# Kernel optimization log

Hardware: AMD Instinct MI355X
Metric: run time of the kernel (lower is better)

The kernel has to match this reference:

```python
import jax, jax.numpy as jnp
import numpy as np

HEAD_DIM = 64
AGGR = 4  # attn_aggr_ratio
BN_EPS = 1e-5


def _conv1x1(x, W, b=None):
    # x: [N, Cin, L], W: [Cout, Cin] -> [N, Cout, L]
    y = jnp.einsum('ncl,oc->nol', x, W)
    if b is not None:
        y = y + b[None, :, None]
    return y


def _bn(x, gamma, beta, mean, var):
    # BatchNorm1d, eval mode (running stats). x: [N, C, L]
    inv = gamma * jax.lax.rsqrt(var + BN_EPS)
    return x * inv[None, :, None] + (beta - mean * inv)[None, :, None]


def setup_inputs() -> dict:
    key = jax.random.key(0)
    ks = jax.random.split(key, 8)
    N, C, L = 4, 256, 4096
    s = 1.0 / np.sqrt(C)
    inp = {
        'x': jax.random.normal(ks[0], (N, C, L), jnp.float32),
        'Wq': jax.random.normal(ks[1], (C, C), jnp.float32) * s,
        'bq': jnp.zeros((C,), jnp.float32),
        'Wk': jax.random.normal(ks[2], (C, C), jnp.float32) * s,
        'bk': jnp.zeros((C,), jnp.float32),
        'Wv': jax.random.normal(ks[3], (C, C), jnp.float32) * s,
        'bv': jnp.zeros((C,), jnp.float32),
        'Wo': jax.random.normal(ks[4], (C, C), jnp.float32) * s,
        'bo': jnp.zeros((C,), jnp.float32),
        'Wa': jax.random.normal(ks[5], (C, C), jnp.float32) * s,
        'g1': jnp.ones((C,), jnp.float32), 'b1': jnp.zeros((C,), jnp.float32),
        'm1': jnp.zeros((C,), jnp.float32), 'v1': jnp.ones((C,), jnp.float32),
        'g2': jnp.ones((C,), jnp.float32), 'b2': jnp.zeros((C,), jnp.float32),
        'm2': jnp.zeros((C,), jnp.float32), 'v2': jnp.ones((C,), jnp.float32),
    }
    return inp


def reference(x, Wq, bq, Wk, bk, Wv, bv, Wo, bo, Wa,
              g1, b1, m1, v1, g2, b2, m2, v2):
    N, C, L = x.shape
    H, E = C // HEAD_DIM, HEAD_DIM
    # q projection on full-resolution input
    q = _conv1x1(x, Wq, bq).reshape(N, H, E, L)
    # LocalAwareAggregationBlock: avg+max pool (kernel=AGGR, L divisible), 1x1 conv, BN
    xp = x.reshape(N, C, L // AGGR, AGGR)
    xa = xp.mean(axis=-1) + xp.max(axis=-1)          # [N, C, L//AGGR]
    xa = _conv1x1(xa, Wa)                             # bias=False
    xa = _bn(xa, g1, b1, m1, v1)
    # post-aggregation norm
    xa = _bn(xa, g2, b2, m2, v2)
    k = _conv1x1(xa, Wk, bk).reshape(N, H, E, -1)     # [N, H, E, L2]
    v = _conv1x1(xa, Wv, bv).reshape(N, H, E, -1)
    # attention: softmax((q/sqrt(E))^T k) @ v^T
    scale = 1.0 / np.sqrt(E)
    scores = jnp.einsum('nhel,nhem->nhlm', q * scale, k)  # [N, H, L, L2]
    attn = jax.nn.softmax(scores, axis=-1)
    o = jnp.einsum('nhlm,nhem->nhel', attn, v).reshape(N, C, L)
    return _conv1x1(o, Wo, bo)
```

## Files before the change

### kernel.cpp

```cpp
#include <hip/hip_runtime.h>
#include <stdint.h>

constexpr int NBATCH = 4;
constexpr int CH     = 256;
constexpr int LEN    = 4096;
constexpr int LPOOL  = 1024;
constexpr int NH     = 4;
constexpr int HD     = 64;

typedef __attribute__((ext_vector_type(8))) short short8;
typedef __attribute__((ext_vector_type(4))) float float4e;
typedef __attribute__((ext_vector_type(16))) float float16e;
typedef __attribute__((ext_vector_type(2))) unsigned uint2v;

__device__ __forceinline__ unsigned short f2bf(float f) {
    union { unsigned int i; float f; } v; v.f = f;
    unsigned int lsb = (v.i >> 16) & 1u;
    v.i += 0x7fffu + lsb;
    return (unsigned short)(v.i >> 16);
}
__device__ __forceinline__ unsigned pack2bf(float lo, float hi) {
    unsigned a = __float_as_uint(lo) + 0x8000u;
    unsigned b = __float_as_uint(hi) + 0x8000u;
    return __builtin_amdgcn_perm(b, a, 0x07060302u);
}
__device__ __forceinline__ float fast_exp2(float x) {
#if __has_builtin(__builtin_amdgcn_exp2f)
    return __builtin_amdgcn_exp2f(x);
#else
    float r;
    asm("v_exp_f32 %0, %1" : "=v"(r) : "v"(x));
    return r;
#endif
}
__device__ __forceinline__ void gload16(const void* g, void* l) {
    __builtin_amdgcn_global_load_lds(
        (const __attribute__((address_space(1))) unsigned int*)g,
        (__attribute__((address_space(3))) unsigned int*)l, 16, 0, 0);
}

__global__ __launch_bounds__(256) void transpool_setup(
    const float* __restrict__ x, unsigned short* __restrict__ xbf,
    unsigned short* __restrict__ poolT,
    const float* __restrict__ w0, const float* __restrict__ w1,
    const float* __restrict__ w2, const float* __restrict__ w3,
    const float* __restrict__ w4, unsigned short* __restrict__ outW,
    const float* __restrict__ g1, const float* __restrict__ b1,
    const float* __restrict__ m1, const float* __restrict__ v1,
    const float* __restrict__ g2, const float* __restrict__ b2,
    const float* __restrict__ m2, const float* __restrict__ v2,
    float* __restrict__ scale, float* __restrict__ shift,
    const float* __restrict__ bk, const float* __restrict__ bv,
    float* __restrict__ bkv)
{
    __shared__ float T[64][65];
    __shared__ float P16[64][17];
    int b = blockIdx.x, t = threadIdx.x;
    if (b >= 1024) {
        int sb = b - 1024;
        if (sb < 320) {
            int gid = sb * 256 + t;
            int w = gid >> 14;
            int off = (gid & 16383) * 4;
            const float* src = (w == 0) ? w0 : (w == 1) ? w1 : (w == 2) ? w2 : (w == 3) ? w3 : w4;
            float4 v = *(const float4*)(src + off);
            uint2 pk;
            pk.x = pack2bf(v.x, v.y);
            pk.y = pack2bf(v.z, v.w);
            *(uint2*)(outW + w * 65536 + off) = pk;
        } else {
            float inv1 = g1[t] * rsqrtf(v1[t] + 1e-5f);
            float inv2 = g2[t] * rsqrtf(v2[t] + 1e-5f);
            scale[t] = inv1 * inv2;
            shift[t] = (b1[t] - m1[t] * inv1) * inv2 + (b2[t] - m2[t] * inv2);
            bkv[t] = bk[t];
            bkv[256 + t] = bv[t];
        }
        return;
    }
    int n = b >> 8, c0 = ((b >> 6) & 3) * 64, l0 = (b & 63) * 64;
    const float* xp = x + ((size_t)n * CH + c0) * LEN + l0;
    #pragma unroll
    for (int i = 0; i < 4; i++) {
        int idx = t + i * 256;
        int c = idx >> 4, l4 = idx & 15;
        float4 v = *(const float4*)(xp + (size_t)c * LEN + l4 * 4);
        T[c][l4 * 4 + 0] = v.x; T[c][l4 * 4 + 1] = v.y;
        T[c][l4 * 4 + 2] = v.z; T[c][l4 * 4 + 3] = v.w;
        P16[c][l4] = (v.x + v.y + v.z + v.w) * 0.25f
                   + fmaxf(fmaxf(v.x, v.y), fmaxf(v.z, v.w));
    }
    __syncthreads();
    unsigned short* op = xbf + ((size_t)n * LEN + l0) * CH + c0;
    #pragma unroll
    for (int i = 0; i < 4; i++) {
        int idx = t + i * 256;
        int l = idx >> 4, c4 = idx & 15;
        uint2 pk;
        pk.x = pack2bf(T[c4 * 4 + 0][l], T[c4 * 4 + 1][l]);
        pk.y = pack2bf(T[c4 * 4 + 2][l], T[c4 * 4 + 3][l]);
        *(uint2*)(op + (size_t)l * CH + c4 * 4) = pk;
    }
    int p0 = l0 >> 2;
    #pragma unroll
    for (int k = 0; k < 2; k++) {
        int p = (t >> 5) + k * 8;
        int c2 = (t & 31) * 2;
        unsigned pk = pack2bf(P16[c2][p], P16[c2 + 1][p]);
        *(unsigned*)(poolT + ((size_t)n * LPOOL + p0 + p) * CH + c0 + c2) = pk;
    }
}

__global__ __launch_bounds__(256) void gemm_mfma(
    const unsigned short* __restrict__ A,
    const unsigned short* __restrict__ B, size_t bBatch,
    const float* __restrict__ biasRow,
    const float* __restrict__ scale, const float* __restrict__ shift,
    float* __restrict__ outF, size_t oFBatch,
    unsigned short* __restrict__ out1, size_t o1Batch, int cs1,
    unsigned short* __restrict__ out2, size_t o2Batch, int rs2, int rowSplit,
    int NN, float outScale)
{
    __shared__ unsigned short smem[2 * 128 * 72];
    unsigned short* As = smem;
    unsigned short* Bs = smem + 128 * 72;

    int n = blockIdx.z;
    int t = threadIdx.x;
    int wave = t >> 6, lane = t & 63, m = lane & 15, quad = lane >> 4;
    int wm = wave & 1, wn = wave >> 1;
    int rowTile = blockIdx.y * 128;
    int col0 = blockIdx.x * 128;

    const unsigned short* Ab = A + (size_t)rowTile * 256;
    const unsigned short* Bb = B + (size_t)n * bBatch + (size_t)col0 * 256;

    float4e acc[4][4] = {};

    for (int kk = 0; kk < 256; kk += 64) {
        #pragma unroll
        for (int i = 0; i < 4; i++) {
            int idx = t + i * 256;
            int row = idx >> 3, ch = idx & 7;
            *(uint4*)&As[row * 72 + ch * 8] = *(const uint4*)(Ab + (size_t)row * 256 + kk + ch * 8);
            *(uint4*)&Bs[row * 72 + ch * 8] = *(const uint4*)(Bb + (size_t)row * 256 + kk + ch * 8);
        }
        __syncthreads();
        #pragma unroll
        for (int kc = 0; kc < 2; kc++) {
            short8 af[4], bfr[4];
            #pragma unroll
            for (int i = 0; i < 4; i++)
                af[i] = *(const short8*)&As[(wm * 64 + i * 16 + m) * 72 + kc * 32 + quad * 8];
            #pragma unroll
            for (int j = 0; j < 4; j++)
                bfr[j] = *(const short8*)&Bs[(wn * 64 + j * 16 + m) * 72 + kc * 32 + quad * 8];
            #pragma unroll
            for (int i = 0; i < 4; i++)
                #pragma unroll
                for (int j = 0; j < 4; j++)
                    acc[i][j] = __builtin_amdgcn_mfma_f32_16x16x32_bf16(af[i], bfr[j], acc[i][j], 0, 0, 0);
        }
        __syncthreads();
    }

    if (outF) {
        float* TOf = (float*)smem;
        float* dst = outF + (size_t)n * oFBatch;
        #pragma unroll
        for (int half = 0; half < 2; half++) {
            __syncthreads();
            if (wm == half) {
                #pragma unroll
                for (int i = 0; i < 4; i++) {
                    int rowL = i * 16 + quad * 4;
                    int rowG = rowTile + half * 64 + rowL;
                    float br[4], sc[4], sh[4];
                    #pragma unroll
                    for (int r = 0; r < 4; r++) {
                        br[r] = biasRow ? biasRow[rowG + r] : 0.0f;
                        sc[r] = scale ? scale[rowG + r] : 1.0f;
                        sh[r] = shift ? shift[rowG + r] : 0.0f;
                    }
                    #pragma unroll
                    for (int j = 0; j < 4; j++) {
                        int colL = wn * 64 + j * 16 + m;
                        float4e c = acc[i][j];
                        #pragma unroll
                        for (int r = 0; r < 4; r++)
                            TOf[(rowL + r) * 128 + colL] = ((c[r] + br[r]) * sc[r] + sh[r]) * outScale;
                    }
                }
            }
            __syncthreads();
            #pragma unroll
            for (int w = 0; w < 8; w++) {
                int idx = t + w * 256;
                int row = idx >> 5, c4 = idx & 31;
                *(float4*)(dst + (size_t)(rowTile + half * 64 + row) * NN + col0 + c4 * 4) =
                    *(const float4*)&TOf[row * 128 + c4 * 4];
            }
        }
        return;
    }

    bool mode2 = (rowTile >= rowSplit);
    unsigned short* TO = smem;
    #pragma unroll
    for (int i = 0; i < 4; i++) {
        int rowL = wm * 64 + i * 16 + quad * 4;
        int rowG = rowTile + rowL;
        float br[4], sc[4], sh[4];
        #pragma unroll
        for (int r = 0; r < 4; r++) {
            br[r] = biasRow ? biasRow[rowG + r] : 0.0f;
            sc[r] = scale ? scale[rowG + r] : 1.0f;
            sh[r] = shift ? shift[rowG + r] : 0.0f;
        }
        #pragma unroll
        for (int j = 0; j < 4; j++) {
            int colL = wn * 64 + j * 16 + m;
            float4e c = acc[i][j];
            float v0 = ((c[0] + br[0]) * sc[0] + sh[0]) * outScale;
            float v1 = ((c[1] + br[1]) * sc[1] + sh[1]) * outScale;
            float v2 = ((c[2] + br[2]) * sc[2] + sh[2]) * outScale;
            float v3 = ((c[3] + br[3]) * sc[3] + sh[3]) * outScale;
            if (!mode2) {
                uint2 pk;
                pk.x = pack2bf(v0, v1);
                pk.y = pack2bf(v2, v3);
                *(uint2*)&TO[colL * 136 + rowL] = pk;
            } else {
                TO[(rowL + 0) * 136 + colL] = f2bf(v0);
                TO[(rowL + 1) * 136 + colL] = f2bf(v1);
                TO[(rowL + 2) * 136 + colL] = f2bf(v2);
                TO[(rowL + 3) * 136 + colL] = f2bf(v3);
            }
        }
    }
    __syncthreads();
    if (!mode2) {
        unsigned short* dst = out1 + (size_t)n * o1Batch;
        #pragma unroll
        for (int w = 0; w < 8; w++) {
            int idx = t + w * 256;
            int l = idx >> 4, ch = idx & 15;
            *(uint4*)(dst + (size_t)(col0 + l) * cs1 + rowTile + ch * 8) =
                *(const uint4*)&TO[l * 136 + ch * 8];
        }
    } else {
        unsigned short* dst = out2 + (size_t)n * o2Batch;
        int rowBase = rowTile - rowSplit;
        #pragma unroll
        for (int w = 0; w < 8; w++) {
            int idx = t + w * 256;
            int row = idx >> 4, ch = idx & 15;
            *(uint4*)(dst + (size_t)(rowBase + row) * rs2 + col0 + ch * 8) =
                *(const uint4*)&TO[row * 136 + ch * 8];
        }
    }
}

__global__ __launch_bounds__(256, 2) void attn_mfma(
    const unsigned short* __restrict__ Qb,
    const unsigned short* __restrict__ Kb,
    const unsigned short* __restrict__ Vb,
    unsigned short* __restrict__ Obf)
{
    __shared__ unsigned short Ks[2][64 * 64];
    __shared__ unsigned short Vs[2][64 * 64];

    int qb = blockIdx.x;
    int h  = blockIdx.y;
    int n  = blockIdx.z;
    int t  = threadIdx.x;
    int wave = t >> 6, lane = t & 63;
    int col = lane & 31;
    int hi  = lane >> 5;
    int l0 = qb * 128 + wave * 32;

    const unsigned short* qp = Qb + ((size_t)n * LEN + l0 + col) * CH + h * HD + hi * 8;
    short8 bQ[4];
    #pragma unroll
    for (int dc = 0; dc < 4; dc++)
        bQ[dc] = *(const short8*)(qp + dc * 16);

    float16e Oa[2];
    #pragma unroll
    for (int e = 0; e < 2; e++)
        #pragma unroll
        for (int r = 0; r < 16; r++) Oa[e][r] = 0.0f;
    float l_run = 0.0f;

    const unsigned short* KgBase = Kb + (size_t)n * LPOOL * CH + h * HD;
    const unsigned short* VgBase = Vb + ((size_t)n * CH + h * HD) * LPOOL;
    const float NEG = -17.312340f;

    int srow[2], schs[2], ldsb[2];
    #pragma unroll
    for (int i = 0; i < 2; i++) {
        int idx = t + i * 256;
        srow[i] = idx >> 3;
        schs[i] = (idx & 7) ^ (srow[i] & 7);
        ldsb[i] = wave * 1024 + i * 4096;
    }
    int ldoff[2][4];
    #pragma unroll
    for (int g = 0; g < 2; g++)
        #pragma unroll
        for (int c = 0; c < 4; c++) {
            int row = g * 32 + col;
            ldoff[g][c] = row * 128 + ((c * 32 + hi * 16) ^ ((row & 7) << 4));
        }

    #pragma unroll
    for (int i = 0; i < 2; i++) {
        gload16(KgBase + (size_t)srow[i] * CH + schs[i] * 8, (char*)Ks[0] + ldsb[i]);
        gload16(VgBase + (size_t)srow[i] * LPOOL + schs[i] * 8, (char*)Vs[0] + ldsb[i]);
    }

    #pragma unroll 2
    for (int kt = 0; kt < 16; kt++) {
        int cur = kt & 1;
        asm volatile("s_waitcnt vmcnt(0)" ::: "memory");
        __builtin_amdgcn_sched_barrier(0);
        __builtin_amdgcn_s_barrier();
        __builtin_amdgcn_sched_barrier(0);
        if (kt < 15) {
            int nxt = cur ^ 1;
            const unsigned short* ksrc = KgBase + (size_t)(kt + 1) * 64 * CH;
            const unsigned short* vsrc = VgBase + (kt + 1) * 64;
            #pragma unroll
            for (int i = 0; i < 2; i++) {
                gload16(ksrc + (size_t)srow[i] * CH + schs[i] * 8, (char*)Ks[nxt] + ldsb[i]);
                gload16(vsrc + (size_t)srow[i] * LPOOL + schs[i] * 8, (char*)Vs[nxt] + ldsb[i]);
            }
        }

        const char* KsC = (const char*)Ks[cur];
        const char* VsC = (const char*)Vs[cur];
        #pragma unroll
        for (int kh = 0; kh < 2; kh++) {
            float16e c;
            #pragma unroll
            for (int r = 0; r < 16; r++) c[r] = NEG;
            __builtin_amdgcn_s_setprio(1);
            #pragma unroll
            for (int dc = 0; dc < 4; dc++) {
                short8 a = *(const short8*)(KsC + ldoff[kh][dc]);
                c = __builtin_amdgcn_mfma_f32_32x32x16_bf16(a, bQ[dc], c, 0, 0, 0);
            }
            __builtin_amdgcn_s_setprio(0);
            float p[16];
            #pragma unroll
            for (int r = 0; r < 16; r++) p[r] = fast_exp2(c[r]);
            l_run += ((p[0] + p[1]) + (p[2] + p[3])) + ((p[4] + p[5]) + (p[6] + p[7]))
                   + ((p[8] + p[9]) + (p[10] + p[11])) + ((p[12] + p[13]) + (p[14] + p[15]));
            union { unsigned u[4]; short8 s; } bP[2];
            #pragma unroll
            for (int kc2 = 0; kc2 < 2; kc2++) {
                int rb = kc2 * 8;
                unsigned A0 = pack2bf(p[rb + 0], p[rb + 1]);
                unsigned B0 = pack2bf(p[rb + 4], p[rb + 5]);
                unsigned A1 = pack2bf(p[rb + 2], p[rb + 3]);
                unsigned B1 = pack2bf(p[rb + 6], p[rb + 7]);
                uint2v s0 = __builtin_amdgcn_permlane32_swap(A0, B0, false, false);
                uint2v s1 = __builtin_amdgcn_permlane32_swap(A1, B1, false, false);
                bP[kc2].u[0] = s0[0];
                bP[kc2].u[1] = s1[0];
                bP[kc2].u[2] = s0[1];
                bP[kc2].u[3] = s1[1];
            }
            __builtin_amdgcn_s_setprio(1);
            #pragma unroll
            for (int eh = 0; eh < 2; eh++)
                #pragma unroll
                for (int kc2 = 0; kc2 < 2; kc2++) {
                    short8 av = *(const short8*)(VsC + ldoff[eh][kh * 2 + kc2]);
                    Oa[eh] = __builtin_amdgcn_mfma_f32_32x32x16_bf16(av, bP[kc2].s, Oa[eh], 0, 0, 0);
                }
            __builtin_amdgcn_s_setprio(0);
        }
    }

    float l = l_run + __shfl_xor(l_run, 32);
    float inv = 1.0f / l;
    unsigned short* op = Obf + ((size_t)n * LEN + l0 + col) * CH + h * HD + hi * 4;
    #pragma unroll
    for (int eh = 0; eh < 2; eh++)
        #pragma unroll
        for (int rq = 0; rq < 4; rq++) {
            int r = rq * 4;
            uint2 pk;
            pk.x = pack2bf(Oa[eh][r + 0] * inv, Oa[eh][r + 1] * inv);
            pk.y = pack2bf(Oa[eh][r + 2] * inv, Oa[eh][r + 3] * inv);
            *(uint2*)(op + eh * 32 + rq * 8) = pk;
        }
}

extern "C" void kernel_launch(void* const* d_in, const int* in_sizes, int n_in,
                              void* d_out, int out_size, void* d_ws, size_t ws_size,
                              hipStream_t stream)
{
    const float* x  = (const float*)d_in[0];
    const float* Wq = (const float*)d_in[1];
    const float* bq = (const float*)d_in[2];
    const float* Wk = (const float*)d_in[3];
    const float* bk = (const float*)d_in[4];
    const float* Wv = (const float*)d_in[5];
    const float* bv = (const float*)d_in[6];
    const float* Wo = (const float*)d_in[7];
    const float* bo = (const float*)d_in[8];
    const float* Wa = (const float*)d_in[9];
    const float* g1 = (const float*)d_in[10];
    const float* b1 = (const float*)d_in[11];
    const float* m1 = (const float*)d_in[12];
    const float* v1 = (const float*)d_in[13];
    const float* g2 = (const float*)d_in[14];
    const float* b2 = (const float*)d_in[15];
    const float* m2 = (const float*)d_in[16];
    const float* v2 = (const float*)d_in[17];

    float* wsf      = (float*)d_ws;
    float* bn_scale = wsf;
    float* bn_shift = wsf + 256;
    float* bkv      = wsf + 512;
    unsigned short* Wbf   = (unsigned short*)(wsf + 1024);
    unsigned short* xbf   = Wbf + 5 * 65536;
    unsigned short* poolT = xbf   + (size_t)NBATCH * LEN * CH;
    unsigned short* xabf  = poolT + (size_t)NBATCH * LPOOL * CH;
    unsigned short* Kbf   = xabf  + (size_t)NBATCH * LPOOL * CH;
    unsigned short* Vbf   = Kbf   + (size_t)NBATCH * LPOOL * CH;
    unsigned short* Qbf   = Vbf   + (size_t)NBATCH * LPOOL * CH;
    unsigned short* Obf   = Qbf   + (size_t)NBATCH * LEN * CH;

    transpool_setup<<<1345, 256, 0, stream>>>(x, xbf, poolT,
        Wq, Wk, Wv, Wo, Wa, Wbf,
        g1, b1, m1, v1, g2, b2, m2, v2, bn_scale, bn_shift, bk, bv, bkv);

    gemm_mfma<<<dim3(32, 2, 4), 256, 0, stream>>>(
        Wbf + 0 * 65536, xbf, (size_t)LEN * CH, bq, nullptr, nullptr,
        nullptr, 0, Qbf, (size_t)LEN * CH, 256, nullptr, 0, 0, 1 << 30,
        LEN, 0.18033688f);

    gemm_mfma<<<dim3(8, 2, 4), 256, 0, stream>>>(
        Wbf + 4 * 65536, poolT, (size_t)LPOOL * CH, nullptr, bn_scale, bn_shift,
        nullptr, 0, xabf, (size_t)LPOOL * CH, 256, nullptr, 0, 0, 1 << 30,
        LPOOL, 1.0f);

    gemm_mfma<<<dim3(8, 4, 4), 256, 0, stream>>>(
        Wbf + 1 * 65536, xabf, (size_t)LPOOL * CH, bkv, nullptr, nullptr,
        nullptr, 0, Kbf, (size_t)LPOOL * CH, 256, Vbf, (size_t)LPOOL * CH, LPOOL, 256,
        LPOOL, 1.0f);

    attn_mfma<<<dim3(LEN / 128, NH, NBATCH), 256, 0, stream>>>(Qbf, Kbf, Vbf, Obf);

    gemm_mfma<<<dim3(32, 2, 4), 256, 0, stream>>>(
        Wbf + 3 * 65536, Obf, (size_t)LEN * CH, bo, nullptr, nullptr,
        (float*)d_out, (size_t)CH * LEN, nullptr, 0, 0, nullptr, 0, 0, 1 << 30,
        LEN, 1.0f);
}
```

Baseline: 168.8 us.

## Double-buffer GEMM with direct global-to-LDS loads and smaller 64-row tiles

Rewrites the projection GEMM kernel to use 64x128 output tiles instead of 128x128 and doubles the grid's row dimension. The K loop is double-buffered: it issues direct global-to-LDS loads for the next K slice while MFMAs run on the current one, and raises wave priority around the MFMA block. It also uses occupancy hint 2 and a dedicated output staging buffer. The aim is to hide global load latency and give more blocks for better CU fill. In exchange the LDS rows are unpadded, which may cause bank conflicts, and each B tile is reused across fewer rows.

Result: faster. 158.8 us (-6.0%).

```diff
diff --git a/kernel.cpp b/kernel.cpp
--- a/kernel.cpp
+++ b/kernel.cpp
@@ -111,7 +111,7 @@
     }
 }
 
-__global__ __launch_bounds__(256) void gemm_mfma(
+__global__ __launch_bounds__(256, 2) void gemm_mfma(
     const unsigned short* __restrict__ A,
     const unsigned short* __restrict__ B, size_t bBatch,
     const float* __restrict__ biasRow,
@@ -121,94 +121,140 @@
     unsigned short* __restrict__ out2, size_t o2Batch, int rs2, int rowSplit,
     int NN, float outScale)
 {
-    __shared__ unsigned short smem[2 * 128 * 72];
-    unsigned short* As = smem;
-    unsigned short* Bs = smem + 128 * 72;
+    __shared__ unsigned short As[2][64 * 64];
+    __shared__ unsigned short Bs[2][128 * 64];
+    __shared__ unsigned short TO[128 * 72];
 
     int n = blockIdx.z;
     int t = threadIdx.x;
     int wave = t >> 6, lane = t & 63, m = lane & 15, quad = lane >> 4;
     int wm = wave & 1, wn = wave >> 1;
-    int rowTile = blockIdx.y * 128;
+    int rowTile = blockIdx.y * 64;
     int col0 = blockIdx.x * 128;
 
     const unsigned short* Ab = A + (size_t)rowTile * 256;
     const unsigned short* Bb = B + (size_t)n * bBatch + (size_t)col0 * 256;
 
-    float4e acc[4][4] = {};
-
-    for (int kk = 0; kk < 256; kk += 64) {
-        #pragma unroll
-        for (int i = 0; i < 4; i++) {
-            int idx = t + i * 256;
-            int row = idx >> 3, ch = idx & 7;
-            *(uint4*)&As[row * 72 + ch * 8] = *(const uint4*)(Ab + (size_t)row * 256 + kk + ch * 8);
-            *(uint4*)&Bs[row * 72 + ch * 8] = *(const uint4*)(Bb + (size_t)row * 256 + kk + ch * 8);
-        }
-        __syncthreads();
+    float4e acc[2][4] = {};
+
+    int arow[2], ach[2];
+    #pragma unroll
+    for (int i = 0; i < 2; i++) {
+        int idx = t + i * 256;
+        arow[i] = idx >> 3;
+        ach[i]  = idx & 7;
+    }
+    int brow[4], bch[4];
+    #pragma unroll
+    for (int i = 0; i < 4; i++) {
+        int idx = t + i * 256;
+        brow[i] = idx >> 3;
+        bch[i]  = idx & 7;
+    }
+    int ldsW[4];
+    #pragma unroll
+    for (int i = 0; i < 4; i++) ldsW[i] = wave * 1024 + i * 4096;
+
+    int aoff[2][2], boff[4][2];
+    #pragma unroll
+    for (int i = 0; i < 2; i++) {
+        int r = wm * 32 + i * 16 + m;
+        #pragma unroll
+        for (int kc = 0; kc < 2; kc++)
+            aoff[i][kc] = r * 128 + kc * 64 + quad * 16;
+    }
+    #pragma unroll
+    for (int j = 0; j < 4; j++) {
+        int r = wn * 64 + j * 16 + m;
+        #pragma unroll
+        for (int kc = 0; kc < 2; kc++)
+            boff[j][kc] = r * 128 + kc * 64 + quad * 16;
+    }
+
+    #pragma unroll
+    for (int i = 0; i < 2; i++)
+        gload16(Ab + (size_t)arow[i] * 256 + ach[i] * 8, (char*)As[0] + ldsW[i]);
+    #pragma unroll
+    for (int i = 0; i < 4; i++)
+        gload16(Bb + (size_t)brow[i] * 256 + bch[i] * 8, (char*)Bs[0] + ldsW[i]);
+
+    #pragma unroll
+    for (int s = 0; s < 4; s++) {
+        int cur = s & 1;
+        asm volatile("s_waitcnt vmcnt(0)" ::: "memory");
+        __builtin_amdgcn_sched_barrier(0);
+        __builtin_amdgcn_s_barrier();
+        __builtin_amdgcn_sched_barrier(0);
+        if (s < 3) {
+            int nxt = cur ^ 1;
+            int kk = (s + 1) * 64;
+            #pragma unroll
+            for (int i = 0; i < 2; i++)
+                gload16(Ab + (size_t)arow[i] * 256 + kk + ach[i] * 8, (char*)As[nxt] + ldsW[i]);
+            #pragma unroll
+            for (int i = 0; i < 4; i++)
+                gload16(Bb + (size_t)brow[i] * 256 + kk + bch[i] * 8, (char*)Bs[nxt] + ldsW[i]);
+        }
+        const char* AsC = (const char*)As[cur];
+        const char* BsC = (const char*)Bs[cur];
         #pragma unroll
         for (int kc = 0; kc < 2; kc++) {
-            short8 af[4], bfr[4];
-            #pragma unroll
-            for (int i = 0; i < 4; i++)
-                af[i] = *(const short8*)&As[(wm * 64 + i * 16 + m) * 72 + kc * 32 + quad * 8];
+            short8 af[2], bfr[4];
+            #pragma unroll
+            for (int i = 0; i < 2; i++)
+                af[i] = *(const short8*)(AsC + aoff[i][kc]);
             #pragma unroll
             for (int j = 0; j < 4; j++)
-                bfr[j] = *(const short8*)&Bs[(wn * 64 + j * 16 + m) * 72 + kc * 32 + quad * 8];
-            #pragma unroll
-            for (int i = 0; i < 4; i++)
+                bfr[j] = *(const short8*)(BsC + boff[j][kc]);
+            __builtin_amdgcn_s_setprio(1);
+            #pragma unroll
+            for (int i = 0; i < 2; i++)
                 #pragma unroll
                 for (int j = 0; j < 4; j++)
                     acc[i][j] = __builtin_amdgcn_mfma_f32_16x16x32_bf16(af[i], bfr[j], acc[i][j], 0, 0, 0);
+            __builtin_amdgcn_s_setprio(0);
+        }
+    }
+    __syncthreads();
+
+    if (outF) {
+        float* TOf = (float*)Bs;
+        float* dst = outF + (size_t)n * oFBatch;
+        #pragma unroll
+        for (int i = 0; i < 2; i++) {
+            int rowL = wm * 32 + i * 16 + quad * 4;
+            int rowG = rowTile + rowL;
+            float br[4], sc[4], sh[4];
+            #pragma unroll
+            for (int r = 0; r < 4; r++) {
+                br[r] = biasRow ? biasRow[rowG + r] : 0.0f;
+                sc[r] = scale ? scale[rowG + r] : 1.0f;
+                sh[r] = shift ? shift[rowG + r] : 0.0f;
+            }
+            #pragma unroll
+            for (int j = 0; j < 4; j++) {
+                int colL = wn * 64 + j * 16 + m;
+                float4e c = acc[i][j];
+                #pragma unroll
+                for (int r = 0; r < 4; r++)
+                    TOf[(rowL + r) * 128 + colL] = ((c[r] + br[r]) * sc[r] + sh[r]) * outScale;
+            }
         }
         __syncthreads();
-    }
-
-    if (outF) {
-        float* TOf = (float*)smem;
-        float* dst = outF + (size_t)n * oFBatch;
-        #pragma unroll
-        for (int half = 0; half < 2; half++) {
-            __syncthreads();
-            if (wm == half) {
-                #pragma unroll
-                for (int i = 0; i < 4; i++) {
-                    int rowL = i * 16 + quad * 4;
-                    int rowG = rowTile + half * 64 + rowL;
-                    float br[4], sc[4], sh[4];
-                    #pragma unroll
-                    for (int r = 0; r < 4; r++) {
-                        br[r] = biasRow ? biasRow[rowG + r] : 0.0f;
-                        sc[r] = scale ? scale[rowG + r] : 1.0f;
-                        sh[r] = shift ? shift[rowG + r] : 0.0f;
-                    }
-                    #pragma unroll
-                    for (int j = 0; j < 4; j++) {
-                        int colL = wn * 64 + j * 16 + m;
-                        float4e c = acc[i][j];
-                        #pragma unroll
-                        for (int r = 0; r < 4; r++)
-                            TOf[(rowL + r) * 128 + colL] = ((c[r] + br[r]) * sc[r] + sh[r]) * outScale;
-                    }
-                }
-            }
-            __syncthreads();
-            #pragma unroll
-            for (int w = 0; w < 8; w++) {
-                int idx = t + w * 256;
-                int row = idx >> 5, c4 = idx & 31;
-                *(float4*)(dst + (size_t)(rowTile + half * 64 + row) * NN + col0 + c4 * 4) =
-                    *(const float4*)&TOf[row * 128 + c4 * 4];
-            }
+        #pragma unroll
+        for (int w = 0; w < 8; w++) {
+            int idx = t + w * 256;
+            int row = idx >> 5, c4 = idx & 31;
+            *(float4*)(dst + (size_t)(rowTile + row) * NN + col0 + c4 * 4) =
+                *(const float4*)&TOf[row * 128 + c4 * 4];
         }
         return;
     }
 
     bool mode2 = (rowTile >= rowSplit);
-    unsigned short* TO = smem;
-    #pragma unroll
-    for (int i = 0; i < 4; i++) {
-        int rowL = wm * 64 + i * 16 + quad * 4;
+    #pragma unroll
+    for (int i = 0; i < 2; i++) {
+        int rowL = wm * 32 + i * 16 + quad * 4;
         int rowG = rowTile + rowL;
         float br[4], sc[4], sh[4];
         #pragma unroll
@@ -229,7 +275,7 @@
                 uint2 pk;
                 pk.x = pack2bf(v0, v1);
                 pk.y = pack2bf(v2, v3);
-                *(uint2*)&TO[colL * 136 + rowL] = pk;
+                *(uint2*)&TO[colL * 72 + rowL] = pk;
             } else {
                 TO[(rowL + 0) * 136 + colL] = f2bf(v0);
                 TO[(rowL + 1) * 136 + colL] = f2bf(v1);
@@ -242,17 +288,17 @@
     if (!mode2) {
         unsigned short* dst = out1 + (size_t)n * o1Batch;
         #pragma unroll
-        for (int w = 0; w < 8; w++) {
+        for (int w = 0; w < 4; w++) {
             int idx = t + w * 256;
-            int l = idx >> 4, ch = idx & 15;
+            int l = idx >> 3, ch = idx & 7;
             *(uint4*)(dst + (size_t)(col0 + l) * cs1 + rowTile + ch * 8) =
-                *(const uint4*)&TO[l * 136 + ch * 8];
+                *(const uint4*)&TO[l * 72 + ch * 8];
         }
     } else {
         unsigned short* dst = out2 + (size_t)n * o2Batch;
         int rowBase = rowTile - rowSplit;
         #pragma unroll
-        for (int w = 0; w < 8; w++) {
+        for (int w = 0; w < 4; w++) {
             int idx = t + w * 256;
             int row = idx >> 4, ch = idx & 15;
             *(uint4*)(dst + (size_t)(rowBase + row) * rs2 + col0 + ch * 8) =
@@ -438,24 +484,24 @@
         Wq, Wk, Wv, Wo, Wa, Wbf,
         g1, b1, m1, v1, g2, b2, m2, v2, bn_scale, bn_shift, bk, bv, bkv);
 
-    gemm_mfma<<<dim3(32, 2, 4), 256, 0, stream>>>(
+    gemm_mfma<<<dim3(32, 4, 4), 256, 0, stream>>>(
         Wbf + 0 * 65536, xbf, (size_t)LEN * CH, bq, nullptr, nullptr,
         nullptr, 0, Qbf, (size_t)LEN * CH, 256, nullptr, 0, 0, 1 << 30,
         LEN, 0.18033688f);
 
-    gemm_mfma<<<dim3(8, 2, 4), 256, 0, stream>>>(
+    gemm_mfma<<<dim3(8, 4, 4), 256, 0, stream>>>(
         Wbf + 4 * 65536, poolT, (size_t)LPOOL * CH, nullptr, bn_scale, bn_shift,
         nullptr, 0, xabf, (size_t)LPOOL * CH, 256, nullptr, 0, 0, 1 << 30,
         LPOOL, 1.0f);
 
-    gemm_mfma<<<dim3(8, 4, 4), 256, 0, stream>>>(
+    gemm_mfma<<<dim3(8, 8, 4), 256, 0, stream>>>(
         Wbf + 1 * 65536, xabf, (size_t)LPOOL * CH, bkv, nullptr, nullptr,
         nullptr, 0, Kbf, (size_t)LPOOL * CH, 256, Vbf, (size_t)LPOOL * CH, LPOOL, 256,
         LPOOL, 1.0f);
 
     attn_mfma<<<dim3(LEN / 128, NH, NBATCH), 256, 0, stream>>>(Qbf, Kbf, Vbf, Obf);
 
-    gemm_mfma<<<dim3(32, 2, 4), 256, 0, stream>>>(
+    gemm_mfma<<<dim3(32, 4, 4), 256, 0, stream>>>(
         Wbf + 3 * 65536, Obf, (size_t)LEN * CH, bo, nullptr, nullptr,
         (float*)d_out, (size_t)CH * LEN, nullptr, 0, 0, nullptr, 0, 0, 1 << 30,
         LEN, 1.0f);
```
